# Kernel tuning notes

Hardware: AMD Instinct MI355X
Metric: run time of the kernel (lower is better)

The kernel has to match this reference:

```python
import jax, jax.numpy as jnp
import numpy as np

B, TXT, IMG, D, H = 1, 512, 2048, 1024, 16
HD = D // H
MLP = 4 * D
L = TXT + IMG

def _ln(x, s, b, eps=1e-6):
    mu = jnp.mean(x, -1, keepdims=True)
    var = jnp.var(x, -1, keepdims=True)
    return (x - mu) * jax.lax.rsqrt(var + eps) * s + b

def _rms(x, scale, eps=1e-6):
    return x * jax.lax.rsqrt(jnp.mean(x * x, -1, keepdims=True) + eps) * scale

def _rope(x, pe):
    # x: [B,H,L,HD] -> pairs [B,H,L,HD/2,1,2]; pe: [1,1,L,HD/2,2,2]
    xr = x.reshape(x.shape[0], x.shape[1], x.shape[2], -1, 1, 2)
    out = pe[..., 0] * xr[..., 0] + pe[..., 1] * xr[..., 1]
    return out.reshape(x.shape)

def _mod(vec, w, b):
    m = jax.nn.silu(vec) @ w + b  # [B, 6D]
    return jnp.split(m[:, None, :], 6, axis=-1)

def _stream_qkv(x, shift, scale, n1s, n1b, qkv_w, qkv_b, qs, ks):
    xm = (1 + scale) * _ln(x, n1s, n1b) + shift
    qkv = xm @ qkv_w + qkv_b  # [B,L,3D]
    b_, l_ = qkv.shape[0], qkv.shape[1]
    qkv = qkv.reshape(b_, l_, 3, H, HD).transpose(2, 0, 3, 1, 4)  # 'B L (K H D) -> K B H L D'
    q, k, v = qkv[0], qkv[1], qkv[2]
    return _rms(q, qs), _rms(k, ks), v

def _fwd(img, txt, vec, pe,
         img_mod_w, img_mod_b, img_norm1_s, img_norm1_b, img_qkv_w, img_qkv_b,
         img_qscale, img_kscale, img_proj_w, img_proj_b, img_norm2_s, img_norm2_b,
         img_mlp_w1, img_mlp_b1, img_mlp_w2, img_mlp_b2,
         txt_mod_w, txt_mod_b, txt_norm1_s, txt_norm1_b, txt_qkv_w, txt_qkv_b,
         txt_qscale, txt_kscale, txt_proj_w, txt_proj_b, txt_norm2_s, txt_norm2_b,
         txt_mlp_w1, txt_mlp_b1, txt_mlp_w2, txt_mlp_b2):
    i_sh1, i_sc1, i_g1, i_sh2, i_sc2, i_g2 = _mod(vec, img_mod_w, img_mod_b)
    t_sh1, t_sc1, t_g1, t_sh2, t_sc2, t_g2 = _mod(vec, txt_mod_w, txt_mod_b)
    iq, ik, iv = _stream_qkv(img, i_sh1, i_sc1, img_norm1_s, img_norm1_b, img_qkv_w, img_qkv_b, img_qscale, img_kscale)
    tq, tk, tv = _stream_qkv(txt, t_sh1, t_sc1, txt_norm1_s, txt_norm1_b, txt_qkv_w, txt_qkv_b, txt_qscale, txt_kscale)
    q = jnp.concatenate((tq, iq), axis=2)  # txt tokens first
    k = jnp.concatenate((tk, ik), axis=2)
    v = jnp.concatenate((tv, iv), axis=2)
    q = _rope(q, pe)
    k = _rope(k, pe)
    logits = jnp.einsum('bhqd,bhkd->bhqk', q, k) * (HD ** -0.5)
    attn = jnp.einsum('bhqk,bhkd->bhqd', jax.nn.softmax(logits, axis=-1), v)
    attn = attn.transpose(0, 2, 1, 3).reshape(q.shape[0], L, D)  # 'B H L D -> B L (H D)'
    t_attn, i_attn = attn[:, :TXT], attn[:, TXT:]
    img = img + i_g1 * (i_attn @ img_proj_w + img_proj_b)
    h = (1 + i_sc2) * _ln(img, img_norm2_s, img_norm2_b) + i_sh2
    img = img + i_g2 * (jax.nn.gelu(h @ img_mlp_w1 + img_mlp_b1) @ img_mlp_w2 + img_mlp_b2)
    txt = txt + t_g1 * (t_attn @ txt_proj_w + txt_proj_b)
    h = (1 + t_sc2) * _ln(txt, txt_norm2_s, txt_norm2_b) + t_sh2
    txt = txt + t_g2 * (jax.nn.gelu(h @ txt_mlp_w1 + txt_mlp_b1) @ txt_mlp_w2 + txt_mlp_b2)
    return img, txt

def setup_inputs():
    key = jax.random.key(0)
    keys = iter(jax.random.split(key, 80))
    def rn(shape, s=0.02):
        return jax.random.normal(next(keys), shape, jnp.float32) * s
    inp = {
        'img': jax.random.normal(next(keys), (B, IMG, D), jnp.float32),
        'txt': jax.random.normal(next(keys), (B, TXT, D), jnp.float32),
        'vec': jax.random.normal(next(keys), (B, D), jnp.float32),
        'pe': jax.random.normal(next(keys), (1, 1, L, HD // 2, 2, 2), jnp.float32),
    }
    for p in ('img', 'txt'):
        inp[p + '_mod_w'] = rn((D, 6 * D)); inp[p + '_mod_b'] = jnp.zeros((6 * D,), jnp.float32)
        inp[p + '_norm1_s'] = jnp.ones((D,), jnp.float32); inp[p + '_norm1_b'] = jnp.zeros((D,), jnp.float32)
        inp[p + '_qkv_w'] = rn((D, 3 * D)); inp[p + '_qkv_b'] = jnp.zeros((3 * D,), jnp.float32)
        inp[p + '_qscale'] = jnp.ones((HD,), jnp.float32); inp[p + '_kscale'] = jnp.ones((HD,), jnp.float32)
        inp[p + '_proj_w'] = rn((D, D)); inp[p + '_proj_b'] = jnp.zeros((D,), jnp.float32)
        inp[p + '_norm2_s'] = jnp.ones((D,), jnp.float32); inp[p + '_norm2_b'] = jnp.zeros((D,), jnp.float32)
        inp[p + '_mlp_w1'] = rn((D, MLP)); inp[p + '_mlp_b1'] = jnp.zeros((MLP,), jnp.float32)
        inp[p + '_mlp_w2'] = rn((MLP, D)); inp[p + '_mlp_b2'] = jnp.zeros((D,), jnp.float32)
    return inp

def reference(img, txt, vec, pe,
              img_mod_w, img_mod_b, img_norm1_s, img_norm1_b, img_qkv_w, img_qkv_b,
              img_qscale, img_kscale, img_proj_w, img_proj_b, img_norm2_s, img_norm2_b,
              img_mlp_w1, img_mlp_b1, img_mlp_w2, img_mlp_b2,
              txt_mod_w, txt_mod_b, txt_norm1_s, txt_norm1_b, txt_qkv_w, txt_qkv_b,
              txt_qscale, txt_kscale, txt_proj_w, txt_proj_b, txt_norm2_s, txt_norm2_b,
              txt_mlp_w1, txt_mlp_b1, txt_mlp_w2, txt_mlp_b2):
    return _fwd(img, txt, vec, pe,
                img_mod_w, img_mod_b, img_norm1_s, img_norm1_b, img_qkv_w, img_qkv_b,
                img_qscale, img_kscale, img_proj_w, img_proj_b, img_norm2_s, img_norm2_b,
                img_mlp_w1, img_mlp_b1, img_mlp_w2, img_mlp_b2,
                txt_mod_w, txt_mod_b, txt_norm1_s, txt_norm1_b, txt_qkv_w, txt_qkv_b,
                txt_qscale, txt_kscale, txt_proj_w, txt_proj_b, txt_norm2_s, txt_norm2_b,
                txt_mlp_w1, txt_mlp_b1, txt_mlp_w2, txt_mlp_b2)
```

## Files before the change

### kernel.cpp

```cpp
#include <hip/hip_runtime.h>
#include <cstdint>
#include <cstddef>

#define DD 1024
#define HD 64
#define NH 16
#define LTXT 512
#define LIMG 2048
#define LTOT 2560
#define DMLP 4096

typedef unsigned short u16;
typedef __attribute__((ext_vector_type(8))) __bf16 bf16x8;
typedef __attribute__((ext_vector_type(4))) float f32x4;

__device__ __forceinline__ u16 f2bf(float f) {
  union { float f; uint32_t u; } v; v.f = f;
  uint32_t r = v.u + 0x7FFFu + ((v.u >> 16) & 1u);
  return (u16)(r >> 16);
}
__device__ __forceinline__ float bf2f(u16 u) {
  union { uint32_t u; float f; } v; v.u = ((uint32_t)u) << 16;
  return v.f;
}
__device__ __forceinline__ uint32_t cvtpk(float lo, float hi) {
  uint32_t r;
  asm("v_cvt_pk_bf16_f32 %0, %1, %2" : "=v"(r) : "v"(lo), "v"(hi));
  return r;
}
__device__ __forceinline__ float geluf(float x) {
  const float u = fmaf(x * x, 0.044715f, 1.0f);
  const float e = __expf(x * u * -1.5957691216057308f);
  return x / (1.f + e);
}
__device__ __forceinline__ void gload16(const void* g, void* l) {
  __builtin_amdgcn_global_load_lds(
      (const __attribute__((address_space(1))) void*)g,
      (__attribute__((address_space(3))) void*)l, 16, 0, 0);
}
#define SWZ(row) (((((row) & 3) | ((((row) >> 3) & 1) << 2)) << 4))

__global__ __launch_bounds__(256) void wcast_all(
    const float* __restrict__ s0, const float* __restrict__ s1,
    const float* __restrict__ s2, const float* __restrict__ s3,
    const float* __restrict__ s4, const float* __restrict__ s5,
    const float* __restrict__ s6, const float* __restrict__ s7,
    u16* __restrict__ d0, u16* __restrict__ d1, u16* __restrict__ d2,
    u16* __restrict__ d3, u16* __restrict__ d4, u16* __restrict__ d5,
    u16* __restrict__ d6, u16* __restrict__ d7) {
  const int b = blockIdx.x;
  const float* W; u16* Wt; int K, N, lb;
  if (b < 768)       { W = s0; Wt = d0; K = 1024; N = 3072; lb = b; }
  else if (b < 1536) { W = s1; Wt = d1; K = 1024; N = 3072; lb = b - 768; }
  else if (b < 1792) { W = s2; Wt = d2; K = 1024; N = 1024; lb = b - 1536; }
  else if (b < 2048) { W = s3; Wt = d3; K = 1024; N = 1024; lb = b - 1792; }
  else if (b < 3072) { W = s4; Wt = d4; K = 1024; N = 4096; lb = b - 2048; }
  else if (b < 4096) { W = s5; Wt = d5; K = 1024; N = 4096; lb = b - 3072; }
  else if (b < 5120) { W = s6; Wt = d6; K = 4096; N = 1024; lb = b - 4096; }
  else               { W = s7; Wt = d7; K = 4096; N = 1024; lb = b - 5120; }
  const int ntn = N >> 6;
  const int n0 = (lb % ntn) * 64, k0 = (lb / ntn) * 64;
  __shared__ float T[64][65];
  const int tx = threadIdx.x & 15, ty = threadIdx.x >> 4;
#pragma unroll
  for (int i = 0; i < 4; ++i) {
    const int r = ty + i * 16;
    const float4 v = *(const float4*)&W[(size_t)(k0 + r) * N + n0 + tx * 4];
    T[r][tx * 4 + 0] = v.x;
    T[r][tx * 4 + 1] = v.y;
    T[r][tx * 4 + 2] = v.z;
    T[r][tx * 4 + 3] = v.w;
  }
  __syncthreads();
  const int rn = threadIdx.x >> 2;
  const int cs = (threadIdx.x & 3) * 16;
  u16 buf[16];
#pragma unroll
  for (int j = 0; j < 16; ++j) buf[j] = f2bf(T[cs + j][rn]);
  u16* dst = &Wt[(size_t)(n0 + rn) * K + k0 + cs];
  *(uint4*)dst = *(uint4*)&buf[0];
  *(uint4*)(dst + 8) = *(uint4*)&buf[8];
}

__global__ __launch_bounds__(256) void mod_gemv_part(
    const float* __restrict__ vec, const float* __restrict__ wi,
    const float* __restrict__ wt, float* __restrict__ part) {
  __shared__ float sv[128];
  const int s = blockIdx.y, kc = blockIdx.z;
  const float* W = s ? wt : wi;
  if (threadIdx.x < 128) {
    float x = vec[kc * 128 + threadIdx.x];
    sv[threadIdx.x] = x / (1.f + __expf(-x));
  }
  __syncthreads();
  const int j = blockIdx.x * 256 + threadIdx.x;
  float acc = 0.f;
#pragma unroll 4
  for (int i = 0; i < 128; ++i)
    acc += sv[i] * W[(size_t)(kc * 128 + i) * 6144 + j];
  part[((size_t)(kc * 2 + s)) * 6144 + j] = acc;
}
__global__ __launch_bounds__(256) void mod_reduce(
    const float* __restrict__ part, const float* __restrict__ bi,
    const float* __restrict__ bt, float* __restrict__ modout) {
  const int idx = blockIdx.x * 256 + threadIdx.x;
  const int s = idx / 6144, j = idx % 6144;
  float a = s ? bt[j] : bi[j];
#pragma unroll
  for (int kc = 0; kc < 8; ++kc) a += part[((size_t)(kc * 2 + s)) * 6144 + j];
  modout[(size_t)s * 6144 + j] = a;
}

__global__ __launch_bounds__(256) void ln_mod2(
    const float* __restrict__ Xtxt, const float* __restrict__ Ximg,
    u16* __restrict__ out, const float* __restrict__ tns,
    const float* __restrict__ tnb, const float* __restrict__ ins,
    const float* __restrict__ inb, const float* __restrict__ modv) {
  __shared__ float red[8];
  const int r = blockIdx.x, tid = threadIdx.x;
  const float* x; const float* ns; const float* nb; const float* mv;
  if (r < LTXT) { x = Xtxt + (size_t)r * DD; ns = tns; nb = tnb; mv = modv + 6144; }
  else { x = Ximg + (size_t)(r - LTXT) * DD; ns = ins; nb = inb; mv = modv; }
  const int c0 = tid * 4;
  const float4 xv = *(const float4*)&x[c0];
  float v[4] = {xv.x, xv.y, xv.z, xv.w};
  float s = 0.f, sq = 0.f;
#pragma unroll
  for (int i = 0; i < 4; ++i) { s += v[i]; sq += v[i] * v[i]; }
#pragma unroll
  for (int o = 32; o; o >>= 1) {
    s += __shfl_xor(s, o);
    sq += __shfl_xor(sq, o);
  }
  if ((tid & 63) == 0) {
    red[tid >> 6] = s;
    red[4 + (tid >> 6)] = sq;
  }
  __syncthreads();
  s = red[0] + red[1] + red[2] + red[3];
  sq = red[4] + red[5] + red[6] + red[7];
  const float mu = s * (1.f / DD);
  const float var = sq * (1.f / DD) - mu * mu;
  const float rstd = rsqrtf(var + 1e-6f);
  const float4 nsv = *(const float4*)&ns[c0];
  const float4 nbv = *(const float4*)&nb[c0];
  const float4 shv = *(const float4*)&mv[c0];
  const float4 scv = *(const float4*)&mv[1024 + c0];
  const float nsa[4] = {nsv.x, nsv.y, nsv.z, nsv.w};
  const float nba[4] = {nbv.x, nbv.y, nbv.z, nbv.w};
  const float sha[4] = {shv.x, shv.y, shv.z, shv.w};
  const float sca[4] = {scv.x, scv.y, scv.z, scv.w};
  ushort4 o4;
  u16 ob[4];
#pragma unroll
  for (int i = 0; i < 4; ++i) {
    const float ln = (v[i] - mu) * rstd * nsa[i] + nba[i];
    ob[i] = f2bf((1.f + sca[i]) * ln + sha[i]);
  }
  o4.x = ob[0]; o4.y = ob[1]; o4.z = ob[2]; o4.w = ob[3];
  *(ushort4*)&out[(size_t)r * DD + c0] = o4;
}

__global__ __launch_bounds__(256) void resid_ln2(
    const float* __restrict__ Xtxt, const float* __restrict__ Ximg,
    const u16* __restrict__ t, const float* __restrict__ modv,
    const float* __restrict__ tns, const float* __restrict__ tnb,
    const float* __restrict__ ins, const float* __restrict__ inb,
    float* __restrict__ otxt, float* __restrict__ oimg,
    u16* __restrict__ hout) {
  __shared__ float red[8];
  const int r = blockIdx.x, tid = threadIdx.x;
  const float* x; const float* ns; const float* nb; const float* mv; float* y;
  if (r < LTXT) {
    x = Xtxt + (size_t)r * DD; ns = tns; nb = tnb; mv = modv + 6144;
    y = otxt + (size_t)r * DD;
  } else {
    x = Ximg + (size_t)(r - LTXT) * DD; ns = ins; nb = inb; mv = modv;
    y = oimg + (size_t)(r - LTXT) * DD;
  }
  const int c0 = tid * 4;
  const float4 xv = *(const float4*)&x[c0];
  const ushort4 tb = *(const ushort4*)&t[(size_t)r * DD + c0];
  const float4 gv = *(const float4*)&mv[2048 + c0];
  float v[4];
  v[0] = xv.x + gv.x * bf2f(tb.x);
  v[1] = xv.y + gv.y * bf2f(tb.y);
  v[2] = xv.z + gv.z * bf2f(tb.z);
  v[3] = xv.w + gv.w * bf2f(tb.w);
  *(float4*)&y[c0] = *(float4*)v;
  float s = 0.f, sq = 0.f;
#pragma unroll
  for (int i = 0; i < 4; ++i) { s += v[i]; sq += v[i] * v[i]; }
#pragma unroll
  for (int o = 32; o; o >>= 1) {
    s += __shfl_xor(s, o);
    sq += __shfl_xor(sq, o);
  }
  if ((tid & 63) == 0) {
    red[tid >> 6] = s;
    red[4 + (tid >> 6)] = sq;
  }
  __syncthreads();
  s = red[0] + red[1] + red[2] + red[3];
  sq = red[4] + red[5] + red[6] + red[7];
  const float mu = s * (1.f / DD);
  const float var = sq * (1.f / DD) - mu * mu;
  const float rstd = rsqrtf(var + 1e-6f);
  const float4 nsv = *(const float4*)&ns[c0];
  const float4 nbv = *(const float4*)&nb[c0];
  const float4 shv = *(const float4*)&mv[3072 + c0];
  const float4 scv = *(const float4*)&mv[4096 + c0];
  const float nsa[4] = {nsv.x, nsv.y, nsv.z, nsv.w};
  const float nba[4] = {nbv.x, nbv.y, nbv.z, nbv.w};
  const float sha[4] = {shv.x, shv.y, shv.z, shv.w};
  const float sca[4] = {scv.x, scv.y, scv.z, scv.w};
  ushort4 o4;
  u16 ob[4];
#pragma unroll
  for (int i = 0; i < 4; ++i) {
    const float ln = (v[i] - mu) * rstd * nsa[i] + nba[i];
    ob[i] = f2bf((1.f + sca[i]) * ln + sha[i]);
  }
  o4.x = ob[0]; o4.y = ob[1]; o4.z = ob[2]; o4.w = ob[3];
  *(ushort4*)&hout[(size_t)r * DD + c0] = o4;
}

__global__ __launch_bounds__(256) void gemm_pipe(
    const u16* __restrict__ A, const u16* __restrict__ BtT,
    const u16* __restrict__ BtI, const float* __restrict__ biasT,
    const float* __restrict__ biasI, u16* __restrict__ C,
    float* __restrict__ Cpart, int K, int Kblk, int N, int gelu) {
  __shared__ __align__(16) u16 As[2][128 * 32];
  __shared__ __align__(16) u16 Bs[2][128 * 32];
  const int tid = threadIdx.x, lane = tid & 63, wave = tid >> 6;
  const int nwg = gridDim.x * gridDim.y;
  const int orig = blockIdx.x + blockIdx.y * gridDim.x;
  const int lb = (orig & 7) * (nwg >> 3) + (orig >> 3);
  const int bn = lb / 20, bm = lb % 20;
  const int kc = blockIdx.z;
  const u16* Bt = (bm < (LTXT / 128)) ? BtT : BtI;
  const int wm = wave >> 1, wn = wave & 1;
  const int lr = lane & 15, lk = lane >> 4;
  f32x4 acc[4][4] = {};
  const size_t a0 = (size_t)bm * 128;
  const size_t b0 = (size_t)bn * 128;
  const int kbase = kc * Kblk;
  const int NT = Kblk >> 5;
  const int srow = lane >> 2, soff = (lane & 3) * 8;

#define STAGE(t, buf)                                                         \
  {                                                                           \
    const int k0_ = kbase + (t) * 32;                                         \
    _Pragma("unroll") for (int j = 0; j < 2; ++j) {                           \
      const int chunk = wave * 2 + j;                                         \
      gload16(&A[(a0 + chunk * 16 + srow) * K + k0_ + soff],                  \
              &As[buf][chunk * 512]);                                         \
      gload16(&Bt[(b0 + chunk * 16 + srow) * K + k0_ + soff],                 \
              &Bs[buf][chunk * 512]);                                         \
    }                                                                         \
  }

  STAGE(0, 0);
  STAGE(1, 1);
  for (int t = 0; t < NT; ++t) {
    if (t + 1 < NT) {
      asm volatile("s_waitcnt vmcnt(4)" ::: "memory");
    } else {
      asm volatile("s_waitcnt vmcnt(0)" ::: "memory");
    }
    __builtin_amdgcn_s_barrier();
    const int b = t & 1;
    bf16x8 af[4], bfv[4];
#pragma unroll
    for (int m = 0; m < 4; ++m)
      af[m] = *(const bf16x8*)&As[b][(wm * 64 + m * 16 + lr) * 32 + lk * 8];
#pragma unroll
    for (int n = 0; n < 4; ++n)
      bfv[n] = *(const bf16x8*)&Bs[b][(wn * 64 + n * 16 + lr) * 32 + lk * 8];
    asm volatile("s_waitcnt lgkmcnt(0)" ::: "memory");
    __builtin_amdgcn_sched_barrier(0);
    __builtin_amdgcn_s_barrier();
    if (t + 2 < NT) STAGE(t + 2, b);
    __builtin_amdgcn_sched_barrier(0);
    __builtin_amdgcn_s_setprio(1);
#pragma unroll
    for (int m = 0; m < 4; ++m)
#pragma unroll
      for (int n = 0; n < 4; ++n)
        acc[m][n] = __builtin_amdgcn_mfma_f32_16x16x32_bf16(af[m], bfv[n],
                                                            acc[m][n], 0, 0, 0);
    __builtin_amdgcn_s_setprio(0);
  }
#undef STAGE

  if (Cpart) {
    float* dst = Cpart + (size_t)kc * ((size_t)LTOT * N);
#pragma unroll
    for (int n = 0; n < 4; ++n) {
      const int col = bn * 128 + wn * 64 + n * 16 + lr;
#pragma unroll
      for (int m = 0; m < 4; ++m)
#pragma unroll
        for (int r = 0; r < 4; ++r) {
          const size_t row = a0 + wm * 64 + m * 16 + lk * 4 + r;
          dst[row * (size_t)N + col] = acc[m][n][r];
        }
    }
  } else {
    const float* bias = (bm < (LTXT / 128)) ? biasT : biasI;
#pragma unroll
    for (int n = 0; n < 4; ++n) {
      const int col = bn * 128 + wn * 64 + n * 16 + lr;
      const float bv = bias[col];
#pragma unroll
      for (int m = 0; m < 4; ++m)
#pragma unroll
        for (int r = 0; r < 4; ++r) {
          const size_t row = a0 + wm * 64 + m * 16 + lk * 4 + r;
          float v = acc[m][n][r] + bv;
          if (gelu) v = geluf(v);
          C[row * (size_t)N + col] = f2bf(v);
        }
    }
  }
}

__global__ __launch_bounds__(256) void gemm_reduce(
    const float* __restrict__ part, const float* __restrict__ bT,
    const float* __restrict__ bI, u16* __restrict__ C, int N, int kcnt) {
  const size_t idx = (size_t)(blockIdx.x * 256 + threadIdx.x) * 4;
  const int row = (int)(idx / N), col = (int)(idx % N);
  float4 a = *(const float4*)&part[idx];
  for (int kc = 1; kc < kcnt; ++kc) {
    const float4 b = *(const float4*)&part[(size_t)kc * LTOT * N + idx];
    a.x += b.x; a.y += b.y; a.z += b.z; a.w += b.w;
  }
  const float* bias = (row < LTXT) ? bT : bI;
  ushort4 o;
  o.x = f2bf(a.x + bias[col]);
  o.y = f2bf(a.y + bias[col + 1]);
  o.z = f2bf(a.z + bias[col + 2]);
  o.w = f2bf(a.w + bias[col + 3]);
  *(ushort4*)&C[idx] = o;
}

__global__ __launch_bounds__(256) void gemm_reduce_gate(
    const float* __restrict__ part, const float* __restrict__ bT,
    const float* __restrict__ bI, const float* __restrict__ modv,
    float* __restrict__ otxt, float* __restrict__ oimg, int kcnt) {
  const size_t idx = (size_t)(blockIdx.x * 256 + threadIdx.x) * 4;
  const int row = (int)(idx >> 10), col = (int)(idx & 1023);
  float4 a = *(const float4*)&part[idx];
  for (int kc = 1; kc < kcnt; ++kc) {
    const float4 b = *(const float4*)&part[(size_t)kc * LTOT * DD + idx];
    a.x += b.x; a.y += b.y; a.z += b.z; a.w += b.w;
  }
  const float* bias; const float* mv; float* o;
  if (row < LTXT) {
    bias = bT; mv = modv + 6144; o = otxt + (size_t)row * DD + col;
  } else {
    bias = bI; mv = modv; o = oimg + (size_t)(row - LTXT) * DD + col;
  }
  const float4 g = *(const float4*)&mv[5120 + col];
  const float4 cur = *(const float4*)o;
  float4 r;
  r.x = cur.x + g.x * (a.x + bias[col]);
  r.y = cur.y + g.y * (a.y + bias[col + 1]);
  r.z = cur.z + g.z * (a.z + bias[col + 2]);
  r.w = cur.w + g.w * (a.w + bias[col + 3]);
  *(float4*)o = r;
}

__global__ __launch_bounds__(256) void scat_rope(
    const u16* __restrict__ qkv, u16* __restrict__ q, u16* __restrict__ k,
    const float* __restrict__ pe, const float* __restrict__ iqs,
    const float* __restrict__ iks, const float* __restrict__ tqs,
    const float* __restrict__ tks) {
  const int gw = (blockIdx.x * 256 + threadIdx.x) >> 6;
  const int lane = threadIdx.x & 63;
  const int l = gw % LTOT, h = gw / LTOT;
  const size_t rb = (size_t)l * 3072 + h * 64 + lane;
  const float qv = bf2f(qkv[rb]);
  const float kv = bf2f(qkv[rb + 1024]);
  const float* qs = (l < LTXT) ? tqs : iqs;
  const float* ks = (l < LTXT) ? tks : iks;
  const float* peb = pe + (size_t)l * 128 + (lane >> 1) * 4 + (lane & 1) * 2;
  const size_t base = ((size_t)h * LTOT + l) * HD + lane;
  {
    float ss = qv * qv;
#pragma unroll
    for (int o = 32; o; o >>= 1) ss += __shfl_xor(ss, o);
    float xn = qv * rsqrtf(ss * (1.f / HD) + 1e-6f) * qs[lane];
    float part = __shfl_xor(xn, 1);
    float x0 = (lane & 1) ? part : xn;
    float x1 = (lane & 1) ? xn : part;
    q[base] = f2bf(peb[0] * x0 + peb[1] * x1);
  }
  {
    float ss = kv * kv;
#pragma unroll
    for (int o = 32; o; o >>= 1) ss += __shfl_xor(ss, o);
    float xn = kv * rsqrtf(ss * (1.f / HD) + 1e-6f) * ks[lane];
    float part = __shfl_xor(xn, 1);
    float x0 = (lane & 1) ? part : xn;
    float x1 = (lane & 1) ? xn : part;
    k[base] = f2bf(peb[0] * x0 + peb[1] * x1);
  }
}

__global__ __launch_bounds__(256) void vt_build(const u16* __restrict__ qkv,
                                                u16* __restrict__ vt) {
  __shared__ u16 T[64][72];
  const int b = blockIdx.x;
  const int h = b & 15, lt = b >> 4;
  const int tid = threadIdx.x;
  const int r = tid >> 3, c8 = (tid & 7) * 8;
  const size_t srcbase = (size_t)(lt * 64) * 3072 + 2048 + h * 64;
  *(uint4*)&T[r][c8] = *(const uint4*)&qkv[srcbase + (size_t)r * 3072 + c8];
  *(uint4*)&T[r + 32][c8] =
      *(const uint4*)&qkv[srcbase + (size_t)(r + 32) * 3072 + c8];
  __syncthreads();
  const int d = tid >> 2, lc = (tid & 3) * 16;
  u16 buf[16];
#pragma unroll
  for (int j = 0; j < 16; ++j) buf[j] = T[lc + j][d];
  u16* dst = &vt[((size_t)h * 64 + d) * LTOT + lt * 64 + lc];
  *(uint4*)dst = *(uint4*)&buf[0];
  *(uint4*)(dst + 8) = *(uint4*)&buf[8];
}

template <int SPLIT>
__global__ __launch_bounds__(512) void attn_mfma(
    const u16* __restrict__ Q, const u16* __restrict__ Kg,
    const u16* __restrict__ VT, u16* __restrict__ out,
    float* __restrict__ part) {
  __shared__ __align__(16) u16 Ks[2][64 * 64];
  __shared__ __align__(16) u16 Vs[2][64 * 64];
  const int tid = threadIdx.x, lane = tid & 63, w = tid >> 6;
  const int lr = lane & 15, lk = lane >> 4;
  const int blk = blockIdx.x;
  const int h = ((blk & 7) << 1) | ((blk >> 3) & 1);
  const int half = (SPLIT == 2) ? ((blk >> 4) & 1) : 0;
  const int q0 = (SPLIT == 2 ? (blk >> 5) : (blk >> 4)) * 128;
  const size_t hb = (size_t)h * LTOT;
  char* KsB0 = (char*)&Ks[0][0];
  char* VsB0 = (char*)&Vs[0][0];

  const int q = q0 + w * 16 + lr;
  const bf16x8 qa0 = *(const bf16x8*)&Q[(hb + q) * HD + lk * 8];
  const bf16x8 qa1 = *(const bf16x8*)&Q[(hb + q) * HD + 32 + lk * 8];

  const int srow = tid >> 3;
  const int soff = tid & 7;
  const int NT = (LTOT / SPLIT) / 64;
  const int kstart = half * (LTOT / 2);

  float m_run = -1e30f, l_run = 0.f;
  f32x4 acc[4] = {};
  uint4 kst, vst;

  kst = *(const uint4*)&Kg[(hb + kstart + srow) * HD + soff * 8];
  vst = *(const uint4*)&VT[((size_t)h * HD + srow) * LTOT + kstart + soff * 8];
  *(uint4*)(KsB0 + ((srow * 128 + soff * 16) ^ SWZ(srow))) = kst;
  *(uint4*)(VsB0 + ((srow * 128 + soff * 16) ^ SWZ(srow))) = vst;
  __syncthreads();

  const float scale = 0.125f;
  for (int t = 0; t < NT; ++t) {
    char* KsC = KsB0 + (t & 1) * 8192;
    char* VsC = VsB0 + (t & 1) * 8192;
    if (t + 1 < NT) {
      const int k0n = kstart + (t + 1) * 64;
      kst = *(const uint4*)&Kg[(hb + k0n + srow) * HD + soff * 8];
      vst = *(const uint4*)&VT[((size_t)h * HD + srow) * LTOT + k0n + soff * 8];
    }
    f32x4 s[4];
    __builtin_amdgcn_s_setprio(1);
#pragma unroll
    for (int g = 0; g < 4; ++g) {
      const int kr = (lr >> 2) * 8 + (g & 1) * 4 + (lr & 3) + (g >> 1) * 32;
      const int sw = SWZ(kr);
      const bf16x8 ka0 = *(const bf16x8*)(KsC + ((kr * 128 + lk * 16) ^ sw));
      const bf16x8 ka1 = *(const bf16x8*)(KsC + ((kr * 128 + 64 + lk * 16) ^ sw));
      f32x4 z = {0.f, 0.f, 0.f, 0.f};
      z = __builtin_amdgcn_mfma_f32_16x16x32_bf16(ka0, qa0, z, 0, 0, 0);
      z = __builtin_amdgcn_mfma_f32_16x16x32_bf16(ka1, qa1, z, 0, 0, 0);
      s[g] = z;
    }
    __builtin_amdgcn_s_setprio(0);
    float tmax = s[0][0];
#pragma unroll
    for (int g = 0; g < 4; ++g)
#pragma unroll
      for (int r = 0; r < 4; ++r) tmax = fmaxf(tmax, s[g][r]);
    tmax = fmaxf(tmax, __shfl_xor(tmax, 16));
    tmax = fmaxf(tmax, __shfl_xor(tmax, 32));
    tmax *= scale;
    if (!__all(tmax <= m_run + 8.f)) {
      const float mnew = fmaxf(m_run, tmax);
      const float alpha = __expf(m_run - mnew);
      l_run *= alpha;
#pragma unroll
      for (int dt = 0; dt < 4; ++dt) {
        acc[dt][0] *= alpha;
        acc[dt][1] *= alpha;
        acc[dt][2] *= alpha;
        acc[dt][3] *= alpha;
      }
      m_run = mnew;
    }
    float p[4][4];
    float psum = 0.f;
#pragma unroll
    for (int g = 0; g < 4; ++g)
#pragma unroll
      for (int r = 0; r < 4; ++r) {
        p[g][r] = __expf(s[g][r] * scale - m_run);
        psum += p[g][r];
      }
    psum += __shfl_xor(psum, 16);
    psum += __shfl_xor(psum, 32);
    l_run += psum;
    union { uint32_t u[4]; bf16x8 v; } pb0, pb1;
    pb0.u[0] = cvtpk(p[0][0], p[0][1]);
    pb0.u[1] = cvtpk(p[0][2], p[0][3]);
    pb0.u[2] = cvtpk(p[1][0], p[1][1]);
    pb0.u[3] = cvtpk(p[1][2], p[1][3]);
    pb1.u[0] = cvtpk(p[2][0], p[2][1]);
    pb1.u[1] = cvtpk(p[2][2], p[2][3]);
    pb1.u[2] = cvtpk(p[3][0], p[3][1]);
    pb1.u[3] = cvtpk(p[3][2], p[3][3]);
    __builtin_amdgcn_s_setprio(1);
#pragma unroll
    for (int dt = 0; dt < 4; ++dt) {
      const int vr = dt * 16 + lr;
      const int sw = SWZ(vr);
      const bf16x8 va0 = *(const bf16x8*)(VsC + ((vr * 128 + lk * 16) ^ sw));
      const bf16x8 va1 = *(const bf16x8*)(VsC + ((vr * 128 + 64 + lk * 16) ^ sw));
      acc[dt] = __builtin_amdgcn_mfma_f32_16x16x32_bf16(va0, pb0.v, acc[dt], 0, 0, 0);
      acc[dt] = __builtin_amdgcn_mfma_f32_16x16x32_bf16(va1, pb1.v, acc[dt], 0, 0, 0);
    }
    __builtin_amdgcn_s_setprio(0);
    if (t + 1 < NT) {
      char* KsN = KsB0 + ((t + 1) & 1) * 8192;
      char* VsN = VsB0 + ((t + 1) & 1) * 8192;
      *(uint4*)(KsN + ((srow * 128 + soff * 16) ^ SWZ(srow))) = kst;
      *(uint4*)(VsN + ((srow * 128 + soff * 16) ^ SWZ(srow))) = vst;
      __syncthreads();
    }
  }
  if (SPLIT == 2) {
    float* pr = part + (((size_t)(half * LTOT) + q) * 16 + h) * 68;
#pragma unroll
    for (int dt = 0; dt < 4; ++dt)
      *(f32x4*)&pr[dt * 16 + lk * 4] = acc[dt];
    if (lk == 0) {
      pr[64] = m_run;
      pr[65] = l_run;
    }
  } else {
    __syncthreads();
    const float inv = 1.f / l_run;
    char* ob = KsB0 + w * 2048;
    const int esw = (lr & 7) << 4;
#pragma unroll
    for (int dt = 0; dt < 4; ++dt) {
      const uint32_t a = cvtpk(acc[dt][0] * inv, acc[dt][1] * inv);
      const uint32_t b2 = cvtpk(acc[dt][2] * inv, acc[dt][3] * inv);
      const int ad = lr * 128 + dt * 32 + lk * 8;
      *(uint32_t*)(ob + (ad ^ esw)) = a;
      *(uint32_t*)(ob + ((ad + 4) ^ esw)) = b2;
    }
    __syncthreads();
    const int row = lane >> 2, ch = lane & 3;
    const int rsw = (row & 7) << 4;
    const uint4 o0 = *(const uint4*)(ob + ((row * 128 + ch * 32) ^ rsw));
    const uint4 o1 = *(const uint4*)(ob + ((row * 128 + ch * 32 + 16) ^ rsw));
    u16* orow = &out[(size_t)(q0 + w * 16 + row) * DD + h * HD + ch * 16];
    *(uint4*)orow = o0;
    *(uint4*)(orow + 8) = o1;
  }
}

__global__ __launch_bounds__(256) void attn_merge(const float* __restrict__ part,
                                                  u16* __restrict__ out) {
  const int idx = blockIdx.x * 256 + threadIdx.x;
  const int d4 = idx & 15, h = (idx >> 4) & 15, q = idx >> 8;
  const size_t base0 = ((size_t)q * 16 + h) * 68;
  const size_t base1 = ((size_t)(LTOT + q) * 16 + h) * 68;
  const float m0 = part[base0 + 64], l0 = part[base0 + 65];
  const float m1 = part[base1 + 64], l1 = part[base1 + 65];
  const float m = fmaxf(m0, m1);
  const float a0 = __expf(m0 - m), a1 = __expf(m1 - m);
  const float inv = 1.f / (l0 * a0 + l1 * a1);
  const float4 x0 = *(const float4*)&part[base0 + d4 * 4];
  const float4 x1 = *(const float4*)&part[base1 + d4 * 4];
  const float s0 = a0 * inv, s1 = a1 * inv;
  uint2 o;
  o.x = cvtpk(x0.x * s0 + x1.x * s1, x0.y * s0 + x1.y * s1);
  o.y = cvtpk(x0.z * s0 + x1.z * s1, x0.w * s0 + x1.w * s1);
  *(uint2*)&out[(size_t)q * DD + h * HD + d4 * 4] = o;
}

__global__ __launch_bounds__(256) void resid_gate(
    const float* __restrict__ xin, const u16* __restrict__ t,
    const float* __restrict__ g, float* __restrict__ out, int n4) {
  const int idx = blockIdx.x * 256 + threadIdx.x;
  if (idx >= n4) return;
  const int col = (idx * 4) & (DD - 1);
  const float4 a = ((const float4*)xin)[idx];
  const ushort4 tb = ((const ushort4*)t)[idx];
  const float4 gg = *(const float4*)&g[col];
  float4 r;
  r.x = a.x + gg.x * bf2f(tb.x);
  r.y = a.y + gg.y * bf2f(tb.y);
  r.z = a.z + gg.z * bf2f(tb.z);
  r.w = a.w + gg.w * bf2f(tb.w);
  ((float4*)out)[idx] = r;
}

extern "C" void kernel_launch(void* const* d_in, const int* in_sizes, int n_in,
                              void* d_out, int out_size, void* d_ws,
                              size_t ws_size, hipStream_t stream) {
  const float* img = (const float*)d_in[0];
  const float* txt = (const float*)d_in[1];
  const float* vec = (const float*)d_in[2];
  const float* pe = (const float*)d_in[3];
  const float* i_mod_w = (const float*)d_in[4];
  const float* i_mod_b = (const float*)d_in[5];
  const float* i_n1s = (const float*)d_in[6];
  const float* i_n1b = (const float*)d_in[7];
  const float* i_qkv_w = (const float*)d_in[8];
  const float* i_qkv_b = (const float*)d_in[9];
  const float* i_qs = (const float*)d_in[10];
  const float* i_ks = (const float*)d_in[11];
  const float* i_proj_w = (const float*)d_in[12];
  const float* i_proj_b = (const float*)d_in[13];
  const float* i_n2s = (const float*)d_in[14];
  const float* i_n2b = (const float*)d_in[15];
  const float* i_w1 = (const float*)d_in[16];
  const float* i_b1 = (const float*)d_in[17];
  const float* i_w2 = (const float*)d_in[18];
  const float* i_b2 = (const float*)d_in[19];
  const float* t_mod_w = (const float*)d_in[20];
  const float* t_mod_b = (const float*)d_in[21];
  const float* t_n1s = (const float*)d_in[22];
  const float* t_n1b = (const float*)d_in[23];
  const float* t_qkv_w = (const float*)d_in[24];
  const float* t_qkv_b = (const float*)d_in[25];
  const float* t_qs = (const float*)d_in[26];
  const float* t_ks = (const float*)d_in[27];
  const float* t_proj_w = (const float*)d_in[28];
  const float* t_proj_b = (const float*)d_in[29];
  const float* t_n2s = (const float*)d_in[30];
  const float* t_n2b = (const float*)d_in[31];
  const float* t_w1 = (const float*)d_in[32];
  const float* t_b1 = (const float*)d_in[33];
  const float* t_w2 = (const float*)d_in[34];
  const float* t_b2 = (const float*)d_in[35];

  const size_t LD = (size_t)LTOT * DD;
  uint8_t* p = (uint8_t*)d_ws;
  float* modb = (float*)p;           p += 64 * 1024;
  float* part = (float*)p;           p += 512 * 1024;
  u16* tqkvT = (u16*)p;              p += (size_t)3072 * 1024 * 2;
  u16* iqkvT = (u16*)p;              p += (size_t)3072 * 1024 * 2;
  u16* tprojT = (u16*)p;             p += (size_t)1024 * 1024 * 2;
  u16* iprojT = (u16*)p;             p += (size_t)1024 * 1024 * 2;
  u16* tw1T = (u16*)p;               p += (size_t)4096 * 1024 * 2;
  u16* iw1T = (u16*)p;               p += (size_t)4096 * 1024 * 2;
  u16* tw2T = (u16*)p;               p += (size_t)1024 * 4096 * 2;
  u16* iw2T = (u16*)p;               p += (size_t)1024 * 4096 * 2;
  u16* actA = (u16*)p;               p += LD * 2;
  u16* actB = (u16*)p;               p += (size_t)LTOT * DMLP * 2;
  u16* actC = (u16*)p;               p += LD * 2 * 3;
  float* gpart = (float*)p;
  const size_t used = (size_t)(p - (uint8_t*)d_ws);
  const size_t avail = ws_size > used ? ws_size - used : 0;
  const size_t attn_part_need = (size_t)2 * LTOT * 16 * 68 * sizeof(float);
  const int attn_split = avail >= attn_part_need ? 2 : 1;
  const int kc_proj = avail >= 2 * LD * sizeof(float) ? 2 : 1;
  const int kc_mlp2 = avail >= 4 * LD * sizeof(float)
                          ? 4
                          : (avail >= 2 * LD * sizeof(float) ? 2 : 1);
  float* out_img = (float*)d_out;
  float* out_txt = out_img + (size_t)LIMG * DD;

  wcast_all<<<6144, 256, 0, stream>>>(t_qkv_w, i_qkv_w, t_proj_w, i_proj_w,
                                      t_w1, i_w1, t_w2, i_w2, tqkvT, iqkvT,
                                      tprojT, iprojT, tw1T, iw1T, tw2T, iw2T);
  mod_gemv_part<<<dim3(24, 2, 8), 256, 0, stream>>>(vec, i_mod_w, t_mod_w, part);
  mod_reduce<<<48, 256, 0, stream>>>(part, i_mod_b, t_mod_b, modb);
  ln_mod2<<<LTOT, 256, 0, stream>>>(txt, img, actA, t_n1s, t_n1b, i_n1s, i_n1b,
                                    modb);
  gemm_pipe<<<dim3(24, 20, 1), 256, 0, stream>>>(actA, tqkvT, iqkvT, t_qkv_b,
                                                 i_qkv_b, actB, nullptr, 1024,
                                                 1024, 3072, 0);
  scat_rope<<<10240, 256, 0, stream>>>(actB, actC, actC + LD, pe, i_qs, i_ks,
                                       t_qs, t_ks);
  vt_build<<<640, 256, 0, stream>>>(actB, actC + 2 * LD);
  if (attn_split == 2) {
    attn_mfma<2><<<640, 512, 0, stream>>>(actC, actC + LD, actC + 2 * LD,
                                          actA, gpart);
    attn_merge<<<2560, 256, 0, stream>>>(gpart, actA);
  } else {
    attn_mfma<1><<<320, 512, 0, stream>>>(actC, actC + LD, actC + 2 * LD, actA,
                                          nullptr);
  }
  if (kc_proj > 1) {
    gemm_pipe<<<dim3(8, 20, kc_proj), 256, 0, stream>>>(
        actA, tprojT, iprojT, nullptr, nullptr, nullptr, gpart, 1024,
        1024 / kc_proj, 1024, 0);
    gemm_reduce<<<2560, 256, 0, stream>>>(gpart, t_proj_b, i_proj_b, actC,
                                          1024, kc_proj);
  } else {
    gemm_pipe<<<dim3(8, 20, 1), 256, 0, stream>>>(actA, tprojT, iprojT,
                                                  t_proj_b, i_proj_b, actC,
                                                  nullptr, 1024, 1024, 1024, 0);
  }
  resid_ln2<<<LTOT, 256, 0, stream>>>(txt, img, actC, modb, t_n2s, t_n2b,
                                      i_n2s, i_n2b, out_txt, out_img,
                                      actC + LD);
  gemm_pipe<<<dim3(32, 20, 1), 256, 0, stream>>>(actC + LD, tw1T, iw1T, t_b1,
                                                 i_b1, actB, nullptr, 1024,
                                                 1024, 4096, 1);
  if (kc_mlp2 > 1) {
    gemm_pipe<<<dim3(8, 20, kc_mlp2), 256, 0, stream>>>(
        actB, tw2T, iw2T, nullptr, nullptr, nullptr, gpart, 4096,
        4096 / kc_mlp2, 1024, 0);
    gemm_reduce_gate<<<2560, 256, 0, stream>>>(gpart, t_b2, i_b2, modb,
                                               out_txt, out_img, kc_mlp2);
  } else {
    gemm_pipe<<<dim3(8, 20, 1), 256, 0, stream>>>(actB, tw2T, iw2T, t_b2, i_b2,
                                                  actC + 2 * LD, nullptr, 4096,
                                                  4096, 1024, 0);
    resid_gate<<<2048, 256, 0, stream>>>(out_img,
                                         actC + 2 * LD + (size_t)LTXT * DD,
                                         modb + 5120, out_img, LIMG * DD / 4);
    resid_gate<<<512, 256, 0, stream>>>(out_txt, actC + 2 * LD,
                                        modb + 6144 + 5120, out_txt,
                                        LTXT * DD / 4);
  }
}
```

Measured before the change: 286.9 us.

## Process two query tiles per wave in attention to reuse K/V LDS reads

The attention kernel now runs 4 waves of 256 threads instead of 8, each wave handling 32 query rows as two 16-row sub-tiles. Each K and V fragment read from shared memory feeds two MFMA chains, halving LDS traffic per unit of compute, and each thread now stages two chunks of the K/V tile. The cost is higher register pressure from doubled accumulators and softmax state, and fewer waves per block to hide latency.

```diff
diff --git a/kernel.cpp b/kernel.cpp
--- a/kernel.cpp
+++ b/kernel.cpp
@@ -430,7 +430,7 @@
 }
 
 template <int SPLIT>
-__global__ __launch_bounds__(512) void attn_mfma(
+__global__ __launch_bounds__(256) void attn_mfma(
     const u16* __restrict__ Q, const u16* __restrict__ Kg,
     const u16* __restrict__ VT, u16* __restrict__ out,
     float* __restrict__ part) {
@@ -446,23 +446,34 @@
   char* KsB0 = (char*)&Ks[0][0];
   char* VsB0 = (char*)&Vs[0][0];
 
-  const int q = q0 + w * 16 + lr;
-  const bf16x8 qa0 = *(const bf16x8*)&Q[(hb + q) * HD + lk * 8];
-  const bf16x8 qa1 = *(const bf16x8*)&Q[(hb + q) * HD + 32 + lk * 8];
-
-  const int srow = tid >> 3;
-  const int soff = tid & 7;
+  const int qA = q0 + w * 32 + lr;
+  const int qB = qA + 16;
+  const bf16x8 qaA0 = *(const bf16x8*)&Q[(hb + qA) * HD + lk * 8];
+  const bf16x8 qaA1 = *(const bf16x8*)&Q[(hb + qA) * HD + 32 + lk * 8];
+  const bf16x8 qaB0 = *(const bf16x8*)&Q[(hb + qB) * HD + lk * 8];
+  const bf16x8 qaB1 = *(const bf16x8*)&Q[(hb + qB) * HD + 32 + lk * 8];
+
   const int NT = (LTOT / SPLIT) / 64;
   const int kstart = half * (LTOT / 2);
 
-  float m_run = -1e30f, l_run = 0.f;
-  f32x4 acc[4] = {};
-  uint4 kst, vst;
-
-  kst = *(const uint4*)&Kg[(hb + kstart + srow) * HD + soff * 8];
-  vst = *(const uint4*)&VT[((size_t)h * HD + srow) * LTOT + kstart + soff * 8];
-  *(uint4*)(KsB0 + ((srow * 128 + soff * 16) ^ SWZ(srow))) = kst;
-  *(uint4*)(VsB0 + ((srow * 128 + soff * 16) ^ SWZ(srow))) = vst;
+  float mA = -1e30f, lA = 0.f, mB = -1e30f, lB = 0.f;
+  f32x4 accA[4] = {}, accB[4] = {};
+  uint4 kst[2], vst[2];
+
+#pragma unroll
+  for (int i = 0; i < 2; ++i) {
+    const int e = tid + i * 256;
+    const int row = e >> 3, soff = e & 7;
+    kst[i] = *(const uint4*)&Kg[(hb + kstart + row) * HD + soff * 8];
+    vst[i] = *(const uint4*)&VT[((size_t)h * HD + row) * LTOT + kstart + soff * 8];
+  }
+#pragma unroll
+  for (int i = 0; i < 2; ++i) {
+    const int e = tid + i * 256;
+    const int row = e >> 3, soff = e & 7;
+    *(uint4*)(KsB0 + ((row * 128 + soff * 16) ^ SWZ(row))) = kst[i];
+    *(uint4*)(VsB0 + ((row * 128 + soff * 16) ^ SWZ(row))) = vst[i];
+  }
   __syncthreads();
 
   const float scale = 0.125f;
@@ -471,10 +482,15 @@
     char* VsC = VsB0 + (t & 1) * 8192;
     if (t + 1 < NT) {
       const int k0n = kstart + (t + 1) * 64;
-      kst = *(const uint4*)&Kg[(hb + k0n + srow) * HD + soff * 8];
-      vst = *(const uint4*)&VT[((size_t)h * HD + srow) * LTOT + k0n + soff * 8];
-    }
-    f32x4 s[4];
+#pragma unroll
+      for (int i = 0; i < 2; ++i) {
+        const int e = tid + i * 256;
+        const int row = e >> 3, soff = e & 7;
+        kst[i] = *(const uint4*)&Kg[(hb + k0n + row) * HD + soff * 8];
+        vst[i] = *(const uint4*)&VT[((size_t)h * HD + row) * LTOT + k0n + soff * 8];
+      }
+    }
+    f32x4 sA[4], sB[4];
     __builtin_amdgcn_s_setprio(1);
 #pragma unroll
     for (int g = 0; g < 4; ++g) {
@@ -482,54 +498,83 @@
       const int sw = SWZ(kr);
       const bf16x8 ka0 = *(const bf16x8*)(KsC + ((kr * 128 + lk * 16) ^ sw));
       const bf16x8 ka1 = *(const bf16x8*)(KsC + ((kr * 128 + 64 + lk * 16) ^ sw));
-      f32x4 z = {0.f, 0.f, 0.f, 0.f};
-      z = __builtin_amdgcn_mfma_f32_16x16x32_bf16(ka0, qa0, z, 0, 0, 0);
-      z = __builtin_amdgcn_mfma_f32_16x16x32_bf16(ka1, qa1, z, 0, 0, 0);
-      s[g] = z;
+      f32x4 zA = {0.f, 0.f, 0.f, 0.f}, zB = {0.f, 0.f, 0.f, 0.f};
+      zA = __builtin_amdgcn_mfma_f32_16x16x32_bf16(ka0, qaA0, zA, 0, 0, 0);
+      zA = __builtin_amdgcn_mfma_f32_16x16x32_bf16(ka1, qaA1, zA, 0, 0, 0);
+      zB = __builtin_amdgcn_mfma_f32_16x16x32_bf16(ka0, qaB0, zB, 0, 0, 0);
+      zB = __builtin_amdgcn_mfma_f32_16x16x32_bf16(ka1, qaB1, zB, 0, 0, 0);
+      sA[g] = zA;
+      sB[g] = zB;
     }
     __builtin_amdgcn_s_setprio(0);
-    float tmax = s[0][0];
+    {
+      float tmax = sA[0][0];
+#pragma unroll
+      for (int g = 0; g < 4; ++g)
+#pragma unroll
+        for (int r = 0; r < 4; ++r) tmax = fmaxf(tmax, sA[g][r]);
+      tmax = fmaxf(tmax, __shfl_xor(tmax, 16));
+      tmax = fmaxf(tmax, __shfl_xor(tmax, 32));
+      tmax *= scale;
+      if (!__all(tmax <= mA + 8.f)) {
+        const float mnew = fmaxf(mA, tmax);
+        const float alpha = __expf(mA - mnew);
+        lA *= alpha;
+#pragma unroll
+        for (int dt = 0; dt < 4; ++dt) {
+          accA[dt][0] *= alpha; accA[dt][1] *= alpha;
+          accA[dt][2] *= alpha; accA[dt][3] *= alpha;
+        }
+        mA = mnew;
+      }
+    }
+    {
+      float tmax = sB[0][0];
+#pragma unroll
+      for (int g = 0; g < 4; ++g)
+#pragma unroll
+        for (int r = 0; r < 4; ++r) tmax = fmaxf(tmax, sB[g][r]);
+      tmax = fmaxf(tmax, __shfl_xor(tmax, 16));
+      tmax = fmaxf(tmax, __shfl_xor(tmax, 32));
+      tmax *= scale;
+      if (!__all(tmax <= mB + 8.f)) {
+        const float mnew = fmaxf(mB, tmax);
+        const float alpha = __expf(mB - mnew);
+        lB *= alpha;
+#pragma unroll
+        for (int dt = 0; dt < 4; ++dt) {
+          accB[dt][0] *= alpha; accB[dt][1] *= alpha;
+          accB[dt][2] *= alpha; accB[dt][3] *= alpha;
+        }
+        mB = mnew;
+      }
+    }
+    float pA[4][4], pB[4][4];
+    float psA = 0.f, psB = 0.f;
 #pragma unroll
     for (int g = 0; g < 4; ++g)
 #pragma unroll
-      for (int r = 0; r < 4; ++r) tmax = fmaxf(tmax, s[g][r]);
-    tmax = fmaxf(tmax, __shfl_xor(tmax, 16));
-    tmax = fmaxf(tmax, __shfl_xor(tmax, 32));
-    tmax *= scale;
-    if (!__all(tmax <= m_run + 8.f)) {
-      const float mnew = fmaxf(m_run, tmax);
-      const float alpha = __expf(m_run - mnew);
-      l_run *= alpha;
-#pragma unroll
-      for (int dt = 0; dt < 4; ++dt) {
-        acc[dt][0] *= alpha;
-        acc[dt][1] *= alpha;
-        acc[dt][2] *= alpha;
-        acc[dt][3] *= alpha;
+      for (int r = 0; r < 4; ++r) {
+        pA[g][r] = __expf(sA[g][r] * scale - mA);
+        psA += pA[g][r];
+        pB[g][r] = __expf(sB[g][r] * scale - mB);
+        psB += pB[g][r];
       }
-      m_run = mnew;
-    }
-    float p[4][4];
-    float psum = 0.f;
-#pragma unroll
-    for (int g = 0; g < 4; ++g)
-#pragma unroll
-      for (int r = 0; r < 4; ++r) {
-        p[g][r] = __expf(s[g][r] * scale - m_run);
-        psum += p[g][r];
-      }
-    psum += __shfl_xor(psum, 16);
-    psum += __shfl_xor(psum, 32);
-    l_run += psum;
-    union { uint32_t u[4]; bf16x8 v; } pb0, pb1;
-    pb0.u[0] = cvtpk(p[0][0], p[0][1]);
-    pb0.u[1] = cvtpk(p[0][2], p[0][3]);
-    pb0.u[2] = cvtpk(p[1][0], p[1][1]);
-    pb0.u[3] = cvtpk(p[1][2], p[1][3]);
-    pb1.u[0] = cvtpk(p[2][0], p[2][1]);
-    pb1.u[1] = cvtpk(p[2][2], p[2][3]);
-    pb1.u[2] = cvtpk(p[3][0], p[3][1]);
-    pb1.u[3] = cvtpk(p[3][2], p[3][3]);
+    psA += __shfl_xor(psA, 16);
+    psA += __shfl_xor(psA, 32);
+    lA += psA;
+    psB += __shfl_xor(psB, 16);
+    psB += __shfl_xor(psB, 32);
+    lB += psB;
+    union { uint32_t u[4]; bf16x8 v; } pA0, pA1, pB0, pB1;
+    pA0.u[0] = cvtpk(pA[0][0], pA[0][1]); pA0.u[1] = cvtpk(pA[0][2], pA[0][3]);
+    pA0.u[2] = cvtpk(pA[1][0], pA[1][1]); pA0.u[3] = cvtpk(pA[1][2], pA[1][3]);
+    pA1.u[0] = cvtpk(pA[2][0], pA[2][1]); pA1.u[1] = cvtpk(pA[2][2], pA[2][3]);
+    pA1.u[2] = cvtpk(pA[3][0], pA[3][1]); pA1.u[3] = cvtpk(pA[3][2], pA[3][3]);
+    pB0.u[0] = cvtpk(pB[0][0], pB[0][1]); pB0.u[1] = cvtpk(pB[0][2], pB[0][3]);
+    pB0.u[2] = cvtpk(pB[1][0], pB[1][1]); pB0.u[3] = cvtpk(pB[1][2], pB[1][3]);
+    pB1.u[0] = cvtpk(pB[2][0], pB[2][1]); pB1.u[1] = cvtpk(pB[2][2], pB[2][3]);
+    pB1.u[2] = cvtpk(pB[3][0], pB[3][1]); pB1.u[3] = cvtpk(pB[3][2], pB[3][3]);
     __builtin_amdgcn_s_setprio(1);
 #pragma unroll
     for (int dt = 0; dt < 4; ++dt) {
@@ -537,48 +582,68 @@
       const int sw = SWZ(vr);
       const bf16x8 va0 = *(const bf16x8*)(VsC + ((vr * 128 + lk * 16) ^ sw));
       const bf16x8 va1 = *(const bf16x8*)(VsC + ((vr * 128 + 64 + lk * 16) ^ sw));
-      acc[dt] = __builtin_amdgcn_mfma_f32_16x16x32_bf16(va0, pb0.v, acc[dt], 0, 0, 0);
-      acc[dt] = __builtin_amdgcn_mfma_f32_16x16x32_bf16(va1, pb1.v, acc[dt], 0, 0, 0);
+      accA[dt] = __builtin_amdgcn_mfma_f32_16x16x32_bf16(va0, pA0.v, accA[dt], 0, 0, 0);
+      accA[dt] = __builtin_amdgcn_mfma_f32_16x16x32_bf16(va1, pA1.v, accA[dt], 0, 0, 0);
+      accB[dt] = __builtin_amdgcn_mfma_f32_16x16x32_bf16(va0, pB0.v, accB[dt], 0, 0, 0);
+      accB[dt] = __builtin_amdgcn_mfma_f32_16x16x32_bf16(va1, pB1.v, accB[dt], 0, 0, 0);
     }
     __builtin_amdgcn_s_setprio(0);
     if (t + 1 < NT) {
       char* KsN = KsB0 + ((t + 1) & 1) * 8192;
       char* VsN = VsB0 + ((t + 1) & 1) * 8192;
-      *(uint4*)(KsN + ((srow * 128 + soff * 16) ^ SWZ(srow))) = kst;
-      *(uint4*)(VsN + ((srow * 128 + soff * 16) ^ SWZ(srow))) = vst;
+#pragma unroll
+      for (int i = 0; i < 2; ++i) {
+        const int e = tid + i * 256;
+        const int row = e >> 3, soff = e & 7;
+        *(uint4*)(KsN + ((row * 128 + soff * 16) ^ SWZ(row))) = kst[i];
+        *(uint4*)(VsN + ((row * 128 + soff * 16) ^ SWZ(row))) = vst[i];
+      }
       __syncthreads();
     }
   }
   if (SPLIT == 2) {
-    float* pr = part + (((size_t)(half * LTOT) + q) * 16 + h) * 68;
-#pragma unroll
-    for (int dt = 0; dt < 4; ++dt)
-      *(f32x4*)&pr[dt * 16 + lk * 4] = acc[dt];
+    float* prA = part + (((size_t)(half * LTOT) + qA) * 16 + h) * 68;
+    float* prB = part + (((size_t)(half * LTOT) + qB) * 16 + h) * 68;
+#pragma unroll
+    for (int dt = 0; dt < 4; ++dt) {
+      *(f32x4*)&prA[dt * 16 + lk * 4] = accA[dt];
+      *(f32x4*)&prB[dt * 16 + lk * 4] = accB[dt];
+    }
     if (lk == 0) {
-      pr[64] = m_run;
-      pr[65] = l_run;
+      prA[64] = mA; prA[65] = lA;
+      prB[64] = mB; prB[65] = lB;
     }
   } else {
     __syncthreads();
-    const float inv = 1.f / l_run;
-    char* ob = KsB0 + w * 2048;
+    const float invA = 1.f / lA, invB = 1.f / lB;
     const int esw = (lr & 7) << 4;
 #pragma unroll
-    for (int dt = 0; dt < 4; ++dt) {
-      const uint32_t a = cvtpk(acc[dt][0] * inv, acc[dt][1] * inv);
-      const uint32_t b2 = cvtpk(acc[dt][2] * inv, acc[dt][3] * inv);
-      const int ad = lr * 128 + dt * 32 + lk * 8;
-      *(uint32_t*)(ob + (ad ^ esw)) = a;
-      *(uint32_t*)(ob + ((ad + 4) ^ esw)) = b2;
+    for (int g = 0; g < 2; ++g) {
+      char* ob = KsB0 + (w * 2 + g) * 2048;
+      const f32x4* ac = g ? accB : accA;
+      const float inv = g ? invB : invA;
+#pragma unroll
+      for (int dt = 0; dt < 4; ++dt) {
+        const uint32_t a = cvtpk(ac[dt][0] * inv, ac[dt][1] * inv);
+        const uint32_t b2 = cvtpk(ac[dt][2] * inv, ac[dt][3] * inv);
+        const int ad = lr * 128 + dt * 32 + lk * 8;
+        *(uint32_t*)(ob + (ad ^ esw)) = a;
+        *(uint32_t*)(ob + ((ad + 4) ^ esw)) = b2;
+      }
     }
     __syncthreads();
     const int row = lane >> 2, ch = lane & 3;
     const int rsw = (row & 7) << 4;
-    const uint4 o0 = *(const uint4*)(ob + ((row * 128 + ch * 32) ^ rsw));
-    const uint4 o1 = *(const uint4*)(ob + ((row * 128 + ch * 32 + 16) ^ rsw));
-    u16* orow = &out[(size_t)(q0 + w * 16 + row) * DD + h * HD + ch * 16];
-    *(uint4*)orow = o0;
-    *(uint4*)(orow + 8) = o1;
+#pragma unroll
+    for (int g = 0; g < 2; ++g) {
+      char* ob = KsB0 + (w * 2 + g) * 2048;
+      const uint4 o0 = *(const uint4*)(ob + ((row * 128 + ch * 32) ^ rsw));
+      const uint4 o1 = *(const uint4*)(ob + ((row * 128 + ch * 32 + 16) ^ rsw));
+      u16* orow =
+          &out[(size_t)(q0 + w * 32 + g * 16 + row) * DD + h * HD + ch * 16];
+      *(uint4*)orow = o0;
+      *(uint4*)(orow + 8) = o1;
+    }
   }
 }
 
@@ -700,11 +765,11 @@
                                        t_qs, t_ks);
   vt_build<<<640, 256, 0, stream>>>(actB, actC + 2 * LD);
   if (attn_split == 2) {
-    attn_mfma<2><<<640, 512, 0, stream>>>(actC, actC + LD, actC + 2 * LD,
+    attn_mfma<2><<<640, 256, 0, stream>>>(actC, actC + LD, actC + 2 * LD,
                                           actA, gpart);
     attn_merge<<<2560, 256, 0, stream>>>(gpart, actA);
   } else {
-    attn_mfma<1><<<320, 512, 0, stream>>>(actC, actC + LD, actC + 2 * LD, actA,
+    attn_mfma<1><<<320, 256, 0, stream>>>(actC, actC + LD, actC + 2 * LD, actA,
                                           nullptr);
   }
   if (kc_proj > 1) {
```

New measurement: 311.1 us. +8.4%, slower.
